# Kernel tuning notes

Measured on AMD Instinct MI355X. Metric: run time of the kernel, lower is better.

Reference implementation:

```python
import jax, jax.numpy as jnp
import numpy as np

V = 200000       # packed vertices across batch of meshes
E = 600000       # packed mesh edges (~3*V)
IMG_FEAT = 960   # sum of resnet18 stage dims 64+128+256+512
H = 128          # hidden_dim
N_REST = 7       # gconv layers after the first (8 total)


def setup_inputs() -> dict:
    key = jax.random.key(0)
    ks = jax.random.split(key, 10)
    w = lambda k, shape: (jax.random.normal(k, shape, jnp.float32) * 0.02)
    return {
        "img_feats": jax.random.normal(ks[0], (V, IMG_FEAT), jnp.float32),
        "verts": jax.random.normal(ks[1], (V, 3), jnp.float32),
        "edges": jax.random.randint(ks[2], (E, 2), 0, V),
        # bottleneck Linear(960 -> 128)
        "bn_W": w(ks[3], (H, IMG_FEAT)), "bn_b": jnp.zeros((H,), jnp.float32),
        # first GraphConv: input_dim = 3 + 128 = 131
        "g0_W0": w(ks[4], (H, H + 3)), "g0_b0": jnp.zeros((H,), jnp.float32),
        "g0_W1": w(ks[5], (H, H + 3)), "g0_b1": jnp.zeros((H,), jnp.float32),
        # remaining 7 GraphConvs (128 -> 128), stacked for lax.scan
        "gW0": w(ks[6], (N_REST, H, H)), "gb0": jnp.zeros((N_REST, H), jnp.float32),
        "gW1": w(ks[7], (N_REST, H, H)), "gb1": jnp.zeros((N_REST, H), jnp.float32),
        # vert_offset Linear(128 -> 3)
        "vo_W": w(ks[8], (3, H)), "vo_b": jnp.zeros((3,), jnp.float32),
    }


def _graph_conv_relu(x, edges, W0, b0, W1, b1):
    """pytorch3d GraphConv (undirected) + ReLU.
    out[i] = w0(x[i]) + sum_{j in N(i)} w1(x[j]); edges aggregated both ways."""
    y0 = x @ W0.T + b0               # [V, H] self term
    y1 = x @ W1.T + b1               # [V, H] neighbor term (bias pre-scatter, as in pytorch3d)
    i, j = edges[:, 0], edges[:, 1]
    agg = jnp.zeros_like(y0).at[i].add(y1[j]).at[j].add(y1[i])
    return jax.nn.relu(y0 + agg)


def reference(img_feats, verts, edges, bn_W, bn_b,
              g0_W0, g0_b0, g0_W1, g0_b1,
              gW0, gb0, gW1, gb1, vo_W, vo_b):
    # bottleneck + ReLU on vert-aligned image features
    h = jax.nn.relu(img_feats @ bn_W.T + bn_b)            # [V, 128]
    x = jnp.concatenate([h, verts], axis=1)               # [V, 131]
    x = _graph_conv_relu(x, edges, g0_W0, g0_b0, g0_W1, g0_b1)

    def step(x, p):
        W0, b0, W1, b1 = p
        return _graph_conv_relu(x, edges, W0, b0, W1, b1), None

    x, _ = jax.lax.scan(step, x, (gW0, gb0, gW1, gb1))    # 7 stacked layers
    delta_v = x @ vo_W.T + vo_b                           # [V, 3]
    return delta_v
```

## Files before the change

kernel.cpp:

```cpp
#include <hip/hip_runtime.h>

#define V_N   200000
#define E_N   600000
#define FEAT  960
#define HDIM  128
#define NREST 7
#define NSCAN 196

typedef __attribute__((ext_vector_type(8))) short bf16x8;
typedef __attribute__((ext_vector_type(4))) float f32x4;

__device__ __forceinline__ unsigned short f2bf(float f) {
    unsigned u = __builtin_bit_cast(unsigned, f);
    unsigned r = (u + 0x7FFFu + ((u >> 16) & 1u)) >> 16;
    return (unsigned short)r;
}
__device__ __forceinline__ float bf2f(unsigned h) {
    unsigned u = h << 16;
    return __builtin_bit_cast(float, u);
}

__device__ __forceinline__ void gload_lds16(const void* g, void* l) {
    __builtin_amdgcn_global_load_lds(
        (const __attribute__((address_space(1))) void*)g,
        (__attribute__((address_space(3))) void*)l, 16, 0, 0);
}

__device__ __forceinline__ void acc8(float* a, uint4 q) {
    a[0] += bf2f(q.x & 0xffffu); a[1] += bf2f(q.x >> 16);
    a[2] += bf2f(q.y & 0xffffu); a[3] += bf2f(q.y >> 16);
    a[4] += bf2f(q.z & 0xffffu); a[5] += bf2f(q.z >> 16);
    a[6] += bf2f(q.w & 0xffffu); a[7] += bf2f(q.w >> 16);
}

template<int KT>
__global__ __launch_bounds__(256) void backbone_mfma_kernel(
    const float* __restrict__ A, int lda,
    const short* __restrict__ B, int ldb,
    const float* __restrict__ bias,
    short* __restrict__ C, int ldc)
{
    __shared__ short Smem[128 * 128];
    short* As = Smem;
    short* Bs = Smem + 128 * 64;
    const int tid = threadIdx.x;
    const int bm0 = blockIdx.x * 128;
    const int wid = tid >> 6, lane = tid & 63;
    const int wm = wid >> 1, wn = wid & 1;
    const int srow = wid * 32 + (lane >> 3);
    const int sc   = lane & 7;

    f32x4 acc[4][4];
    #pragma unroll
    for (int n = 0; n < 4; ++n) {
        float bv = bias[wn * 64 + n * 16 + (lane & 15)];
        #pragma unroll
        for (int m = 0; m < 4; ++m)
            acc[m][n] = (f32x4){bv, bv, bv, bv};
    }

    for (int it = 0; it < KT; ++it) {
        const int k0 = it * 64;
        __syncthreads();
        #pragma unroll
        for (int i = 0; i < 8; ++i) {
            int c = i * 256 + tid;
            int row = c >> 4, c4 = c & 15;
            int grow = bm0 + row; if (grow >= V_N) grow = V_N - 1;
            float4 t = *(const float4*)(A + (size_t)grow * lda + k0 + c4 * 4);
            unsigned lo = (unsigned)f2bf(t.x) | ((unsigned)f2bf(t.y) << 16);
            unsigned hi = (unsigned)f2bf(t.z) | ((unsigned)f2bf(t.w) << 16);
            int e = (row * 64 + c4 * 4) ^ ((row & 7) << 3);
            *(uint2*)&As[e] = make_uint2(lo, hi);
        }
        #pragma unroll
        for (int i = 0; i < 4; ++i) {
            int row = srow + i * 8;
            int g = (sc ^ (row & 7)) << 3;
            gload_lds16(B + (size_t)row * ldb + k0 + g, Bs + (wid * 32 + i * 8) * 64);
        }
        __syncthreads();
        #pragma unroll
        for (int kk = 0; kk < 2; ++kk) {
            bf16x8 a[4], b[4];
            #pragma unroll
            for (int m = 0; m < 4; ++m) {
                int row = wm * 64 + m * 16 + (lane & 15);
                int e = (row * 64 + kk * 32 + (lane >> 4) * 8) ^ ((row & 7) << 3);
                a[m] = *(const bf16x8*)&As[e];
            }
            #pragma unroll
            for (int n = 0; n < 4; ++n) {
                int row = wn * 64 + n * 16 + (lane & 15);
                int e = (row * 64 + kk * 32 + (lane >> 4) * 8) ^ ((row & 7) << 3);
                b[n] = *(const bf16x8*)&Bs[e];
            }
            #pragma unroll
            for (int m = 0; m < 4; ++m)
                #pragma unroll
                for (int n = 0; n < 4; ++n)
                    acc[m][n] = __builtin_amdgcn_mfma_f32_16x16x32_bf16(
                        a[m], b[n], acc[m][n], 0, 0, 0);
        }
    }

    __syncthreads();
    #pragma unroll
    for (int m = 0; m < 4; ++m) {
        #pragma unroll
        for (int j = 0; j < 4; ++j) {
            int row = wm * 64 + m * 16 + (lane >> 4) * 4 + j;
            #pragma unroll
            for (int n = 0; n < 4; ++n) {
                int colx = wn * 64 + n * 16 + (lane & 15);
                float v = fmaxf(acc[m][n][j], 0.f);
                Smem[row * 128 + (((colx >> 3) ^ (row & 7)) << 3) + (colx & 7)] =
                    (short)f2bf(v);
            }
        }
    }
    __syncthreads();
    #pragma unroll
    for (int i = 0; i < 8; ++i) {
        int c = i * 256 + tid;
        int r = c >> 4, c8 = c & 15;
        int grow = bm0 + r;
        if (grow < V_N)
            *(uint4*)&C[(size_t)grow * ldc + c8 * 8] =
                *(const uint4*)&Smem[r * 128 + (c8 ^ (r & 7)) * 8];
    }
}

__global__ __launch_bounds__(256) void agg_sum_kernel(
    const short* __restrict__ x, const int* __restrict__ rowp,
    const int* __restrict__ col, short* __restrict__ s)
{
    int g  = (blockIdx.x * 256 + threadIdx.x) >> 4;
    int il = threadIdx.x & 15;
    if (g >= V_N) return;
    int st = rowp[g], en = rowp[g + 1];
    float a[8] = {0.f, 0.f, 0.f, 0.f, 0.f, 0.f, 0.f, 0.f};
    int p = st;
    for (; p + 4 <= en; p += 4) {
        int u0 = col[p], u1 = col[p + 1], u2 = col[p + 2], u3 = col[p + 3];
        uint4 q0 = *(const uint4*)(x + (size_t)u0 * 128 + il * 8);
        uint4 q1 = *(const uint4*)(x + (size_t)u1 * 128 + il * 8);
        uint4 q2 = *(const uint4*)(x + (size_t)u2 * 128 + il * 8);
        uint4 q3 = *(const uint4*)(x + (size_t)u3 * 128 + il * 8);
        acc8(a, q0); acc8(a, q1); acc8(a, q2); acc8(a, q3);
    }
    if (p + 2 <= en) {
        int u0 = col[p], u1 = col[p + 1];
        uint4 q0 = *(const uint4*)(x + (size_t)u0 * 128 + il * 8);
        uint4 q1 = *(const uint4*)(x + (size_t)u1 * 128 + il * 8);
        acc8(a, q0); acc8(a, q1);
        p += 2;
    }
    if (p < en) {
        uint4 q = *(const uint4*)(x + (size_t)col[p] * 128 + il * 8);
        acc8(a, q);
    }
    uint4 w;
    w.x = (unsigned)f2bf(a[0]) | ((unsigned)f2bf(a[1]) << 16);
    w.y = (unsigned)f2bf(a[2]) | ((unsigned)f2bf(a[3]) << 16);
    w.z = (unsigned)f2bf(a[4]) | ((unsigned)f2bf(a[5]) << 16);
    w.w = (unsigned)f2bf(a[6]) | ((unsigned)f2bf(a[7]) << 16);
    *(uint4*)(s + (size_t)g * 128 + il * 8) = w;
}

template<bool L0>
__global__ __launch_bounds__(256) void gconv_mfma_kernel(
    short* __restrict__ X,
    const short* __restrict__ S,
    const short* __restrict__ B,
    const float* __restrict__ b0, const float* __restrict__ b1,
    const int* __restrict__ deg,
    const float* __restrict__ verts,
    const float* __restrict__ sv,
    const float* __restrict__ Wv)
{
    __shared__ short Smem[128 * 128];
    short* As = Smem;
    short* Bs = Smem + 128 * 64;
    const int tid = threadIdx.x;
    const int bm0 = blockIdx.x * 128;
    const int wid = tid >> 6, lane = tid & 63;
    const int wm = wid >> 1, wn = wid & 1;
    const int srow = wid * 32 + (lane >> 3);
    const int sc   = lane & 7;

    f32x4 acc[4][4] = {};

    for (int it = 0; it < 4; ++it) {
        const short* Ap = (it < 2) ? S : X;
        const int k0 = (it & 1) * 64;
        __syncthreads();
        #pragma unroll
        for (int i = 0; i < 4; ++i) {
            int row = srow + i * 8;
            int g = (sc ^ (row & 7)) << 3;
            int grow = bm0 + row; if (grow >= V_N) grow = V_N - 1;
            gload_lds16(Ap + (size_t)grow * 128 + k0 + g, As + (wid * 32 + i * 8) * 64);
            gload_lds16(B + (size_t)row * 256 + it * 64 + g, Bs + (wid * 32 + i * 8) * 64);
        }
        __syncthreads();
        #pragma unroll
        for (int kk = 0; kk < 2; ++kk) {
            bf16x8 a[4], b[4];
            #pragma unroll
            for (int m = 0; m < 4; ++m) {
                int row = wm * 64 + m * 16 + (lane & 15);
                int e = (row * 64 + kk * 32 + (lane >> 4) * 8) ^ ((row & 7) << 3);
                a[m] = *(const bf16x8*)&As[e];
            }
            #pragma unroll
            for (int n = 0; n < 4; ++n) {
                int row = wn * 64 + n * 16 + (lane & 15);
                int e = (row * 64 + kk * 32 + (lane >> 4) * 8) ^ ((row & 7) << 3);
                b[n] = *(const bf16x8*)&Bs[e];
            }
            #pragma unroll
            for (int m = 0; m < 4; ++m)
                #pragma unroll
                for (int n = 0; n < 4; ++n)
                    acc[m][n] = __builtin_amdgcn_mfma_f32_16x16x32_bf16(
                        a[m], b[n], acc[m][n], 0, 0, 0);
        }
    }

    float bb0[4], bb1[4];
    float w0v[4][3], w1v[4][3];
    #pragma unroll
    for (int n = 0; n < 4; ++n) {
        int colx = wn * 64 + n * 16 + (lane & 15);
        bb0[n] = b0[colx]; bb1[n] = b1[colx];
        if (L0) {
            #pragma unroll
            for (int k = 0; k < 3; ++k) {
                w0v[n][k] = Wv[colx * 8 + k];
                w1v[n][k] = Wv[colx * 8 + 4 + k];
            }
        }
    }

    __syncthreads();
    #pragma unroll
    for (int m = 0; m < 4; ++m) {
        #pragma unroll
        for (int j = 0; j < 4; ++j) {
            int row = wm * 64 + m * 16 + (lane >> 4) * 4 + j;
            int grow = bm0 + row; if (grow >= V_N) grow = V_N - 1;
            float dv = (float)deg[grow];
            float vx = 0.f, vy = 0.f, vz = 0.f;
            float4 s4 = {0.f, 0.f, 0.f, 0.f};
            if (L0) {
                vx = verts[3 * grow]; vy = verts[3 * grow + 1]; vz = verts[3 * grow + 2];
                s4 = *(const float4*)&sv[grow * 4];
            }
            #pragma unroll
            for (int n = 0; n < 4; ++n) {
                int colx = wn * 64 + n * 16 + (lane & 15);
                float v = acc[m][n][j] + bb0[n] + dv * bb1[n];
                if (L0)
                    v += w0v[n][0] * vx + w0v[n][1] * vy + w0v[n][2] * vz
                       + w1v[n][0] * s4.x + w1v[n][1] * s4.y + w1v[n][2] * s4.z;
                v = fmaxf(v, 0.f);
                Smem[row * 128 + (((colx >> 3) ^ (row & 7)) << 3) + (colx & 7)] =
                    (short)f2bf(v);
            }
        }
    }
    __syncthreads();
    #pragma unroll
    for (int i = 0; i < 8; ++i) {
        int c = i * 256 + tid;
        int r = c >> 4, c8 = c & 15;
        int grow = bm0 + r;
        if (grow < V_N)
            *(uint4*)&X[(size_t)grow * 128 + c8 * 8] =
                *(const uint4*)&Smem[r * 128 + (c8 ^ (r & 7)) * 8];
    }
}

__global__ __launch_bounds__(256) void vout_kernel(
    const short* __restrict__ x, const float* __restrict__ W,
    const float* __restrict__ b, float* __restrict__ out)
{
    int w    = (blockIdx.x * blockDim.x + threadIdx.x) >> 6;
    int lane = threadIdx.x & 63;
    int v = w * 2 + (lane >> 5);
    int hl = lane & 31;
    if (v >= V_N) return;
    const unsigned* xr = (const unsigned*)(x + (size_t)v * 128);
    unsigned q0 = xr[hl * 2], q1 = xr[hl * 2 + 1];
    float x0 = bf2f(q0 & 0xffffu), x1 = bf2f(q0 >> 16);
    float x2 = bf2f(q1 & 0xffffu), x3 = bf2f(q1 >> 16);
    int k = hl * 4;
    float a0 = x0 * W[k]       + x1 * W[k + 1]   + x2 * W[k + 2]   + x3 * W[k + 3];
    float a1 = x0 * W[128 + k] + x1 * W[129 + k] + x2 * W[130 + k] + x3 * W[131 + k];
    float a2 = x0 * W[256 + k] + x1 * W[257 + k] + x2 * W[258 + k] + x3 * W[259 + k];
    #pragma unroll
    for (int off = 1; off < 32; off <<= 1) {
        a0 += __shfl_xor(a0, off);
        a1 += __shfl_xor(a1, off);
        a2 += __shfl_xor(a2, off);
    }
    if (hl == 0) {
        out[3 * v]     = a0 + b[0];
        out[3 * v + 1] = a1 + b[1];
        out[3 * v + 2] = a2 + b[2];
    }
}

__global__ __launch_bounds__(256) void prep_all_kernel(
    const float* __restrict__ bnW,
    const float* __restrict__ g0W0, const float* __restrict__ g0W1,
    const float* __restrict__ gW0,  const float* __restrict__ gW1,
    const float* __restrict__ verts,
    const int* __restrict__ rowp, const int* __restrict__ colv,
    short* __restrict__ bnWb, short* __restrict__ Wc,
    float* __restrict__ Wv, float* __restrict__ sv)
{
    int i = blockIdx.x * 256 + threadIdx.x;
    if (i < 128 * FEAT) bnWb[i] = (short)f2bf(bnW[i]);
    if (i < 8 * 128 * 256) {
        int l = i >> 15, r = (i >> 8) & 127, c = i & 255;
        float v;
        if (l == 0)
            v = (c < 128) ? g0W1[r * 131 + c] : g0W0[r * 131 + (c - 128)];
        else {
            int ll = l - 1;
            v = (c < 128) ? gW1[((size_t)ll * 128 + r) * 128 + c]
                          : gW0[((size_t)ll * 128 + r) * 128 + (c - 128)];
        }
        Wc[i] = (short)f2bf(v);
    }
    if (i < 128) {
        Wv[i * 8 + 0] = g0W0[i * 131 + 128];
        Wv[i * 8 + 1] = g0W0[i * 131 + 129];
        Wv[i * 8 + 2] = g0W0[i * 131 + 130];
        Wv[i * 8 + 3] = 0.f;
        Wv[i * 8 + 4] = g0W1[i * 131 + 128];
        Wv[i * 8 + 5] = g0W1[i * 131 + 129];
        Wv[i * 8 + 6] = g0W1[i * 131 + 130];
        Wv[i * 8 + 7] = 0.f;
    }
    if (i < V_N) {
        float sx = 0.f, sy = 0.f, sz = 0.f;
        int en = rowp[i + 1];
        for (int p = rowp[i]; p < en; ++p) {
            int u = colv[p];
            sx += verts[3 * u]; sy += verts[3 * u + 1]; sz += verts[3 * u + 2];
        }
        float4 o = {sx, sy, sz, 0.f};
        *(float4*)&sv[(size_t)i * 4] = o;
    }
}

__global__ void deg_count_kernel(const int* __restrict__ edges, int* __restrict__ deg)
{
    int e = blockIdx.x * blockDim.x + threadIdx.x;
    if (e >= E_N) return;
    int i = edges[2 * e], j = edges[2 * e + 1];
    atomicAdd(&deg[i], 1);
    atomicAdd(&deg[j], 1);
}

__global__ __launch_bounds__(1024) void scan_block_kernel(
    const int* __restrict__ deg, int* __restrict__ excl, int* __restrict__ bsum)
{
    __shared__ int sdata[1024];
    int t = threadIdx.x;
    int base = blockIdx.x * 1024;
    int val = (base + t < V_N) ? deg[base + t] : 0;
    sdata[t] = val; __syncthreads();
    for (int off = 1; off < 1024; off <<= 1) {
        int tmp = (t >= off) ? sdata[t - off] : 0;
        __syncthreads();
        sdata[t] += tmp;
        __syncthreads();
    }
    if (base + t < V_N) excl[base + t] = sdata[t] - val;
    if (t == 1023) bsum[blockIdx.x] = sdata[1023];
}

__global__ __launch_bounds__(256) void scan_bsum_kernel(
    const int* __restrict__ bsum, int* __restrict__ boff)
{
    __shared__ int sdata[256];
    int t = threadIdx.x;
    int val = (t < NSCAN) ? bsum[t] : 0;
    sdata[t] = val; __syncthreads();
    for (int off = 1; off < 256; off <<= 1) {
        int tmp = (t >= off) ? sdata[t - off] : 0;
        __syncthreads();
        sdata[t] += tmp;
        __syncthreads();
    }
    if (t < NSCAN) boff[t] = sdata[t] - val;
    if (t == 255) boff[NSCAN] = sdata[255];
}

__global__ void scan_add_kernel(const int* __restrict__ boff,
                                int* __restrict__ rowp, int* __restrict__ cur)
{
    int i = blockIdx.x * blockDim.x + threadIdx.x;
    if (i < V_N) {
        int r = rowp[i] + boff[i >> 10];
        rowp[i] = r;
        cur[i] = r;
    } else if (i == V_N) {
        rowp[V_N] = boff[NSCAN];
    }
}

__global__ void fill_kernel(const int* __restrict__ edges,
                            int* __restrict__ cur, int* __restrict__ col)
{
    int e = blockIdx.x * blockDim.x + threadIdx.x;
    if (e >= E_N) return;
    int i = edges[2 * e], j = edges[2 * e + 1];
    col[atomicAdd(&cur[i], 1)] = j;
    col[atomicAdd(&cur[j], 1)] = i;
}

extern "C" void kernel_launch(void* const* d_in, const int* in_sizes, int n_in,
                              void* d_out, int out_size, void* d_ws, size_t ws_size,
                              hipStream_t stream)
{
    const float* img   = (const float*)d_in[0];
    const float* verts = (const float*)d_in[1];
    const int*   edges = (const int*)  d_in[2];
    const float* bnW   = (const float*)d_in[3];
    const float* bnb   = (const float*)d_in[4];
    const float* g0W0  = (const float*)d_in[5];
    const float* g0b0  = (const float*)d_in[6];
    const float* g0W1  = (const float*)d_in[7];
    const float* g0b1  = (const float*)d_in[8];
    const float* gW0   = (const float*)d_in[9];
    const float* gb0   = (const float*)d_in[10];
    const float* gW1   = (const float*)d_in[11];
    const float* gb1   = (const float*)d_in[12];
    const float* voW   = (const float*)d_in[13];
    const float* vob   = (const float*)d_in[14];
    float* out = (float*)d_out;

    short* xa   = (short*)d_ws;
    short* sb   = xa   + (size_t)V_N * 128;
    short* bnWb = sb   + (size_t)V_N * 128;
    short* Wc   = bnWb + 128 * FEAT;
    float* Wv   = (float*)(Wc + 8 * 128 * 256);
    float* sv   = Wv   + 128 * 8;
    int*   deg  = (int*)(sv + (size_t)V_N * 4);
    int*   rowp = deg  + V_N;
    int*   cur  = rowp + V_N + 1;
    int*   bsum = cur  + V_N;
    int*   boff = bsum + 256;
    int*   col  = boff + 257;

    hipMemsetAsync(deg, 0, V_N * sizeof(int), stream);
    deg_count_kernel<<<(E_N + 255) / 256, 256, 0, stream>>>(edges, deg);
    scan_block_kernel<<<NSCAN, 1024, 0, stream>>>(deg, rowp, bsum);
    scan_bsum_kernel<<<1, 256, 0, stream>>>(bsum, boff);
    scan_add_kernel<<<(V_N + 256) / 256, 256, 0, stream>>>(boff, rowp, cur);
    fill_kernel<<<(E_N + 255) / 256, 256, 0, stream>>>(edges, cur, col);

    prep_all_kernel<<<(8 * 128 * 256 + 255) / 256, 256, 0, stream>>>(
        bnW, g0W0, g0W1, gW0, gW1, verts, rowp, col, bnWb, Wc, Wv, sv);

    const int MB = (V_N + 127) / 128;
    const int AGGB = (V_N * 16 + 255) / 256;

    backbone_mfma_kernel<15><<<MB, 256, 0, stream>>>(img, FEAT, bnWb, FEAT, bnb, xa, 128);

    agg_sum_kernel<<<AGGB, 256, 0, stream>>>(xa, rowp, col, sb);
    gconv_mfma_kernel<true><<<MB, 256, 0, stream>>>(
        xa, sb, Wc, g0b0, g0b1, deg, verts, sv, Wv);

    for (int l = 1; l <= NREST; ++l) {
        agg_sum_kernel<<<AGGB, 256, 0, stream>>>(xa, rowp, col, sb);
        gconv_mfma_kernel<false><<<MB, 256, 0, stream>>>(
            xa, sb, Wc + (size_t)l * 128 * 256,
            gb0 + (size_t)(l - 1) * 128, gb1 + (size_t)(l - 1) * 128,
            deg, nullptr, nullptr, nullptr);
    }

    vout_kernel<<<(V_N * 32 + 255) / 256, 256, 0, stream>>>(xa, voW, vob, out);
}
```

Measured before the change: 1.042 ms.

## Degree-sort vertices for aggregation and fuse output projection into last gconv

Adds a degree histogram, bin scan and permutation fill so agg_sum processes vertices grouped by degree, which balances the gather loop lengths within a wavefront. Separately, the final graph conv now computes the 128->3 vert-offset projection in its epilogue via shuffles and LDS atomics, so the last bf16 activation write and the separate vout kernel are dropped. The costs are extra preprocessing kernels, an indirect perm lookup that scatters the output writes to sb, and the loss of locality in the gather order.

```diff
diff --git a/kernel.cpp b/kernel.cpp
--- a/kernel.cpp
+++ b/kernel.cpp
@@ -133,12 +133,14 @@
 
 __global__ __launch_bounds__(256) void agg_sum_kernel(
     const short* __restrict__ x, const int* __restrict__ rowp,
-    const int* __restrict__ col, short* __restrict__ s)
+    const int* __restrict__ col, const int* __restrict__ perm,
+    short* __restrict__ s)
 {
     int g  = (blockIdx.x * 256 + threadIdx.x) >> 4;
     int il = threadIdx.x & 15;
     if (g >= V_N) return;
-    int st = rowp[g], en = rowp[g + 1];
+    int v = perm[g];
+    int st = rowp[v], en = rowp[v + 1];
     float a[8] = {0.f, 0.f, 0.f, 0.f, 0.f, 0.f, 0.f, 0.f};
     int p = st;
     for (; p + 4 <= en; p += 4) {
@@ -165,10 +167,10 @@
     w.y = (unsigned)f2bf(a[2]) | ((unsigned)f2bf(a[3]) << 16);
     w.z = (unsigned)f2bf(a[4]) | ((unsigned)f2bf(a[5]) << 16);
     w.w = (unsigned)f2bf(a[6]) | ((unsigned)f2bf(a[7]) << 16);
-    *(uint4*)(s + (size_t)g * 128 + il * 8) = w;
-}
-
-template<bool L0>
+    *(uint4*)(s + (size_t)v * 128 + il * 8) = w;
+}
+
+template<bool L0, bool VOUT>
 __global__ __launch_bounds__(256) void gconv_mfma_kernel(
     short* __restrict__ X,
     const short* __restrict__ S,
@@ -177,7 +179,10 @@
     const int* __restrict__ deg,
     const float* __restrict__ verts,
     const float* __restrict__ sv,
-    const float* __restrict__ Wv)
+    const float* __restrict__ Wv,
+    const float* __restrict__ voW,
+    const float* __restrict__ vob,
+    float* __restrict__ out)
 {
     __shared__ short Smem[128 * 128];
     short* As = Smem;
@@ -243,6 +248,55 @@
         }
     }
 
+    if constexpr (VOUT) {
+        float wv0[4], wv1[4], wv2[4];
+        #pragma unroll
+        for (int n = 0; n < 4; ++n) {
+            int colx = wn * 64 + n * 16 + (lane & 15);
+            wv0[n] = voW[colx]; wv1[n] = voW[128 + colx]; wv2[n] = voW[256 + colx];
+        }
+        __syncthreads();
+        float* vsum = (float*)Smem;
+        for (int q = tid; q < 512; q += 256) vsum[q] = 0.f;
+        __syncthreads();
+        #pragma unroll
+        for (int m = 0; m < 4; ++m) {
+            #pragma unroll
+            for (int j = 0; j < 4; ++j) {
+                int row = wm * 64 + m * 16 + (lane >> 4) * 4 + j;
+                int grow = bm0 + row; if (grow >= V_N) grow = V_N - 1;
+                float dv = (float)deg[grow];
+                float p0 = 0.f, p1 = 0.f, p2 = 0.f;
+                #pragma unroll
+                for (int n = 0; n < 4; ++n) {
+                    float v = fmaxf(acc[m][n][j] + bb0[n] + dv * bb1[n], 0.f);
+                    p0 += v * wv0[n]; p1 += v * wv1[n]; p2 += v * wv2[n];
+                }
+                #pragma unroll
+                for (int off = 1; off < 16; off <<= 1) {
+                    p0 += __shfl_xor(p0, off);
+                    p1 += __shfl_xor(p1, off);
+                    p2 += __shfl_xor(p2, off);
+                }
+                if ((lane & 15) == 0) {
+                    atomicAdd(&vsum[row * 4 + 0], p0);
+                    atomicAdd(&vsum[row * 4 + 1], p1);
+                    atomicAdd(&vsum[row * 4 + 2], p2);
+                }
+            }
+        }
+        __syncthreads();
+        if (tid < 128) {
+            int grow = bm0 + tid;
+            if (grow < V_N) {
+                out[3 * grow]     = vsum[tid * 4]     + vob[0];
+                out[3 * grow + 1] = vsum[tid * 4 + 1] + vob[1];
+                out[3 * grow + 2] = vsum[tid * 4 + 2] + vob[2];
+            }
+        }
+        return;
+    }
+
     __syncthreads();
     #pragma unroll
     for (int m = 0; m < 4; ++m) {
@@ -279,36 +333,6 @@
         if (grow < V_N)
             *(uint4*)&X[(size_t)grow * 128 + c8 * 8] =
                 *(const uint4*)&Smem[r * 128 + (c8 ^ (r & 7)) * 8];
-    }
-}
-
-__global__ __launch_bounds__(256) void vout_kernel(
-    const short* __restrict__ x, const float* __restrict__ W,
-    const float* __restrict__ b, float* __restrict__ out)
-{
-    int w    = (blockIdx.x * blockDim.x + threadIdx.x) >> 6;
-    int lane = threadIdx.x & 63;
-    int v = w * 2 + (lane >> 5);
-    int hl = lane & 31;
-    if (v >= V_N) return;
-    const unsigned* xr = (const unsigned*)(x + (size_t)v * 128);
-    unsigned q0 = xr[hl * 2], q1 = xr[hl * 2 + 1];
-    float x0 = bf2f(q0 & 0xffffu), x1 = bf2f(q0 >> 16);
-    float x2 = bf2f(q1 & 0xffffu), x3 = bf2f(q1 >> 16);
-    int k = hl * 4;
-    float a0 = x0 * W[k]       + x1 * W[k + 1]   + x2 * W[k + 2]   + x3 * W[k + 3];
-    float a1 = x0 * W[128 + k] + x1 * W[129 + k] + x2 * W[130 + k] + x3 * W[131 + k];
-    float a2 = x0 * W[256 + k] + x1 * W[257 + k] + x2 * W[258 + k] + x3 * W[259 + k];
-    #pragma unroll
-    for (int off = 1; off < 32; off <<= 1) {
-        a0 += __shfl_xor(a0, off);
-        a1 += __shfl_xor(a1, off);
-        a2 += __shfl_xor(a2, off);
-    }
-    if (hl == 0) {
-        out[3 * v]     = a0 + b[0];
-        out[3 * v + 1] = a1 + b[1];
-        out[3 * v + 2] = a2 + b[2];
     }
 }
 
@@ -402,13 +426,15 @@
 }
 
 __global__ void scan_add_kernel(const int* __restrict__ boff,
-                                int* __restrict__ rowp, int* __restrict__ cur)
+                                int* __restrict__ rowp, int* __restrict__ cur,
+                                const int* __restrict__ deg, int* __restrict__ hist)
 {
     int i = blockIdx.x * blockDim.x + threadIdx.x;
     if (i < V_N) {
         int r = rowp[i] + boff[i >> 10];
         rowp[i] = r;
         cur[i] = r;
+        atomicAdd(&hist[min(deg[i], 63)], 1);
     } else if (i == V_N) {
         rowp[V_N] = boff[NSCAN];
     }
@@ -422,6 +448,30 @@
     int i = edges[2 * e], j = edges[2 * e + 1];
     col[atomicAdd(&cur[i], 1)] = j;
     col[atomicAdd(&cur[j], 1)] = i;
+}
+
+__global__ void binscan_kernel(const int* __restrict__ hist, int* __restrict__ binptr)
+{
+    __shared__ int sdata[64];
+    int t = threadIdx.x;
+    int val = hist[t];
+    sdata[t] = val; __syncthreads();
+    for (int off = 1; off < 64; off <<= 1) {
+        int tmp = (t >= off) ? sdata[t - off] : 0;
+        __syncthreads();
+        sdata[t] += tmp;
+        __syncthreads();
+    }
+    binptr[t] = sdata[t] - val;
+}
+
+__global__ void permfill_kernel(const int* __restrict__ deg,
+                                int* __restrict__ binptr, int* __restrict__ perm)
+{
+    int v = blockIdx.x * 256 + threadIdx.x;
+    if (v >= V_N) return;
+    int b = min(deg[v], 63);
+    perm[atomicAdd(&binptr[b], 1)] = v;
 }
 
 extern "C" void kernel_launch(void* const* d_in, const int* in_sizes, int n_in,
@@ -452,18 +502,23 @@
     float* Wv   = (float*)(Wc + 8 * 128 * 256);
     float* sv   = Wv   + 128 * 8;
     int*   deg  = (int*)(sv + (size_t)V_N * 4);
-    int*   rowp = deg  + V_N;
+    int*   hist = deg  + V_N;
+    int*   rowp = hist + 64;
     int*   cur  = rowp + V_N + 1;
     int*   bsum = cur  + V_N;
     int*   boff = bsum + 256;
-    int*   col  = boff + 257;
-
-    hipMemsetAsync(deg, 0, V_N * sizeof(int), stream);
+    int*   binp = boff + 257;
+    int*   perm = binp + 64;
+    int*   col  = perm + V_N;
+
+    hipMemsetAsync(deg, 0, (V_N + 64) * sizeof(int), stream);
     deg_count_kernel<<<(E_N + 255) / 256, 256, 0, stream>>>(edges, deg);
     scan_block_kernel<<<NSCAN, 1024, 0, stream>>>(deg, rowp, bsum);
     scan_bsum_kernel<<<1, 256, 0, stream>>>(bsum, boff);
-    scan_add_kernel<<<(V_N + 256) / 256, 256, 0, stream>>>(boff, rowp, cur);
+    scan_add_kernel<<<(V_N + 256) / 256, 256, 0, stream>>>(boff, rowp, cur, deg, hist);
     fill_kernel<<<(E_N + 255) / 256, 256, 0, stream>>>(edges, cur, col);
+    binscan_kernel<<<1, 64, 0, stream>>>(hist, binp);
+    permfill_kernel<<<(V_N + 255) / 256, 256, 0, stream>>>(deg, binp, perm);
 
     prep_all_kernel<<<(8 * 128 * 256 + 255) / 256, 256, 0, stream>>>(
         bnW, g0W0, g0W1, gW0, gW1, verts, rowp, col, bnWb, Wc, Wv, sv);
@@ -473,17 +528,21 @@
 
     backbone_mfma_kernel<15><<<MB, 256, 0, stream>>>(img, FEAT, bnWb, FEAT, bnb, xa, 128);
 
-    agg_sum_kernel<<<AGGB, 256, 0, stream>>>(xa, rowp, col, sb);
-    gconv_mfma_kernel<true><<<MB, 256, 0, stream>>>(
-        xa, sb, Wc, g0b0, g0b1, deg, verts, sv, Wv);
-
-    for (int l = 1; l <= NREST; ++l) {
-        agg_sum_kernel<<<AGGB, 256, 0, stream>>>(xa, rowp, col, sb);
-        gconv_mfma_kernel<false><<<MB, 256, 0, stream>>>(
+    agg_sum_kernel<<<AGGB, 256, 0, stream>>>(xa, rowp, col, perm, sb);
+    gconv_mfma_kernel<true, false><<<MB, 256, 0, stream>>>(
+        xa, sb, Wc, g0b0, g0b1, deg, verts, sv, Wv, nullptr, nullptr, nullptr);
+
+    for (int l = 1; l < NREST; ++l) {
+        agg_sum_kernel<<<AGGB, 256, 0, stream>>>(xa, rowp, col, perm, sb);
+        gconv_mfma_kernel<false, false><<<MB, 256, 0, stream>>>(
             xa, sb, Wc + (size_t)l * 128 * 256,
             gb0 + (size_t)(l - 1) * 128, gb1 + (size_t)(l - 1) * 128,
-            deg, nullptr, nullptr, nullptr);
-    }
-
-    vout_kernel<<<(V_N * 32 + 255) / 256, 256, 0, stream>>>(xa, voW, vob, out);
-}
+            deg, nullptr, nullptr, nullptr, nullptr, nullptr, nullptr);
+    }
+
+    agg_sum_kernel<<<AGGB, 256, 0, stream>>>(xa, rowp, col, perm, sb);
+    gconv_mfma_kernel<false, true><<<MB, 256, 0, stream>>>(
+        xa, sb, Wc + (size_t)NREST * 128 * 256,
+        gb0 + (size_t)(NREST - 1) * 128, gb1 + (size_t)(NREST - 1) * 128,
+        deg, nullptr, nullptr, nullptr, voW, vob, out);
+}
```

Measured after the change: 2.543 ms. 144% more time.
